# Performance work log

Measured on AMD Instinct MI355X. Metric: run time of the kernel, lower is better.

## Reference

```python
import jax, jax.numpy as jnp
from jax import lax
import numpy as np

B, A, N_CLS = 2, 3, 3          # batch, anchors per voxel, classes
D, H, W = 64, 128, 128         # 3D feature-map volume
M = 128                        # padded max GT boxes per sample
ALPHA = 2.0                    # focal exponent (module's self.alpha)
EPS = 1e-4                     # probability clamp (module's self.eps)
NMS = True                     # max-pool NMS filtering on neg mask


def setup_inputs() -> dict:
    key = jax.random.key(0)
    logits = jax.random.normal(key, (B, N_CLS * A, D, H, W), dtype=jnp.float32)
    rng = np.random.default_rng(0)
    # prob_gt: -1 = hard negative to mine, 0 = ignore, c in [1..N_CLS] = positive of class c
    prob = np.zeros((B, A, D, H, W), np.float32)
    prob[rng.random((B, A, D, H, W)) < 0.3] = -1.0
    coord = -np.ones((B, M, 4), np.int64)  # rows (a,d,h,w), -1 padded
    k = 96  # valid GT boxes per sample
    for b in range(B):
        a = rng.integers(0, A, k)
        d = rng.integers(0, D, k)
        h = rng.integers(0, H, k)
        w = rng.integers(0, W, k)
        c = rng.integers(1, N_CLS + 1, k)
        prob[b, a, d, h, w] = c
        coord[b, :k] = np.stack([a, d, h, w], 1)
    return {
        "logits": logits,
        "prob_gt": jnp.asarray(prob),
        "coord_gt": jnp.asarray(coord),
        "weight_cls": jnp.ones((N_CLS,), jnp.float32),
    }


def _per_sample(pp, cg, pg, weight_cls):
    # pp: [N_CLS, A, D, H, W] probs; cg: [M,4] int coords (-1 padded); pg: [A,D,H,W]
    valid = cg[:, 0] > -1                              # [M]
    a = jnp.where(valid, cg[:, 0], 0)
    d = jnp.where(valid, cg[:, 1], 0)
    h = jnp.where(valid, cg[:, 2], 0)
    w = jnp.where(valid, cg[:, 3], 0)
    cls = jnp.where(valid, pg[a, d, h, w].astype(jnp.int32) - 1, 0)  # [M]
    vf = valid.astype(pp.dtype)
    # positive term
    pt = pp[cls, a, d, h, w]                           # [M]
    w_pos = lax.stop_gradient(1.0 - pt) ** ALPHA * weight_cls[cls] * vf
    l_pos = -jnp.sum(jnp.log(pt) * w_pos)
    c_pos = jnp.sum(w_pos)
    # "other classes at positive locations" term
    po = pp[:, a, d, h, w]                             # [N_CLS, M]
    w_oth = lax.stop_gradient(
        jnp.maximum(po - (pt - 0.1)[None, :], 0.0)
        * (po > 0.5) * (pt > 0.5)[None, :]
    )
    # torch `weight[cls_gt] = 0` zeroes whole rows for every gt class present
    zero_rows = jnp.any((jnp.arange(N_CLS)[:, None] == cls[None, :]) & valid[None, :], axis=1)
    w_oth = jnp.where(zero_rows[:, None], 0.0, w_oth) * vf[None, :]
    l_oth = jnp.sum(-jnp.log(1.0 - po) * w_oth)
    c_oth = jnp.sum(w_oth)
    return l_pos, c_pos, l_oth, c_oth


def _focal(logits, prob_gt, coord_gt, weight_cls):
    p = jnp.clip(jax.nn.sigmoid(logits), EPS, 1.0 - EPS)  # [B, N_CLS*A, D, H, W]
    bsz, C, dd, hh, ww = logits.shape
    negmask = (prob_gt == -1).astype(p.dtype)             # [B, A, D, H, W]
    negmask = jnp.repeat(negmask[:, None], N_CLS, axis=1).reshape(p.shape)
    if NMS:
        pooled = lax.reduce_window(logits, -jnp.inf, lax.max,
                                   (1, 1, 3, 3, 3), (1, 1, 1, 1, 1), 'SAME')
        max_filter = lax.stop_gradient((pooled == logits).astype(p.dtype))
        thresh_filter = (p > EPS).astype(p.dtype)
        negmask = negmask * max_filter * thresh_filter
    w_neg = lax.stop_gradient(p) ** ALPHA * negmask
    loss_neg = -jnp.sum(jnp.log(1.0 - p) * w_neg)
    count_neg = jnp.sum(w_neg)
    p6 = p.reshape(bsz, N_CLS, C // N_CLS, dd, hh, ww)
    l_pos, c_pos, l_oth, c_oth = jax.vmap(_per_sample, in_axes=(0, 0, 0, None))(
        p6, coord_gt, prob_gt, weight_cls)
    return jnp.stack([jnp.sum(l_pos), loss_neg, jnp.sum(l_oth),
                      jnp.sum(c_pos), count_neg, jnp.sum(c_oth)])


def reference(logits, prob_gt, coord_gt, weight_cls):
    # returns [cls_loss_pos, cls_loss_neg, cls_loss_other, count_pos, count_neg, count_other]
    return _focal(logits, prob_gt, coord_gt, weight_cls)
```

## Files before the change

kernel.cpp:

```cpp
#include <hip/hip_runtime.h>
#include <cstdint>
#include <cstddef>

#define B_    2
#define A_    3
#define NCLS_ 3
#define CH_   9
#define D_    64
#define H_    128
#define W_    128
#define M_    128
#define TH    16
#define EPS_      1e-4f
#define ONE_M_EPS 0.9999f
#define NLOG2E    -1.4426950408889634f
#define LN2_      0.6931471805599453f

__device__ __forceinline__ float4 fmax4(float4 a, float4 b) {
    return make_float4(fmaxf(a.x, b.x), fmaxf(a.y, b.y),
                       fmaxf(a.z, b.z), fmaxf(a.w, b.w));
}

__device__ __forceinline__ float exp2_fast(float x) { return __builtin_amdgcn_exp2f(x); }
__device__ __forceinline__ float log2_fast(float x) { return __builtin_amdgcn_logf(x); }

__global__ __launch_bounds__(256) void neg_kernel(
    const float* __restrict__ logits, const float* __restrict__ prob,
    float* __restrict__ partials)
{
    const int gh   = blockIdx.x * 8 + (threadIdx.x >> 5);
    const int lw   = threadIdx.x & 31;
    const int lane = threadIdx.x & 63;
    const float NEG = -INFINITY;

    const int d  = gh & (D_ - 1);
    const int ht = (gh >> 6) & (H_ / TH - 1);
    const int bc = gh >> 9;
    const int b  = bc / CH_;
    const int a  = (bc - b * CH_) % A_;

    const size_t HW = (size_t)H_ * W_;
    const float* Ld = logits + ((size_t)bc * D_ + d) * HW + 4 * lw;
    const float* Pb = prob   + (((size_t)b * A_ + a) * D_ + d) * HW + 4 * lw;
    const float* Lm = (d > 0)      ? Ld - HW : Ld;
    const float* Lp = (d + 1 < D_) ? Ld + HW : Ld;
    const int h0 = ht * TH;

    struct Raw { float4 c, m, p; };
    auto issue = [&](int hh) -> Raw {
        const int hc = min(max(hh, 0), H_ - 1);
        const size_t o = (size_t)hc * W_;
        Raw r;
        r.c = *(const float4*)(Ld + o);
        r.m = *(const float4*)(Lm + o);
        r.p = *(const float4*)(Lp + o);
        return r;
    };
    auto ldpg = [&](int hh) -> float4 {
        const int hc = min(hh, H_ - 1);
        return *(const float4*)(Pb + (size_t)hc * W_);
    };

    float lacc2 = 0.0f, cacc = 0.0f;

    Raw rawP = issue(h0 - 1);
    Raw raw0 = issue(h0);
    Raw raw1 = issue(h0 + 1);
    Raw rawD = issue(h0 + 2);
    Raw rawE = issue(h0 + 3);
    float4 pgB = ldpg(h0), pgC = ldpg(h0 + 1);
    float4 pgD = ldpg(h0 + 2), pgE = ldpg(h0 + 3);

    float4 vmA = fmax4(rawP.c, fmax4(rawP.m, rawP.p));
    float4 vmB = fmax4(raw0.c, fmax4(raw0.m, raw0.p));
    float4 xB  = raw0.c;
    float4 vmC = fmax4(raw1.c, fmax4(raw1.m, raw1.p));
    float4 xC  = raw1.c;

    #pragma unroll
    for (int i = 0; i < TH; ++i) {
        const int r = h0 + i;

        Raw rawN; float4 pgN;
        if (i < TH - 4) { rawN = issue(r + 4); pgN = ldpg(r + 4); }

        const float4 vmD = fmax4(rawD.c, fmax4(rawD.m, rawD.p));
        const float4 xD  = rawD.c;

        float4 cm = fmax4(vmA, fmax4(vmB, vmC));
        const float lftv = __shfl(cm.w, (lane + 63) & 63, 64);
        const float rgtv = __shfl(cm.x, (lane + 1) & 63, 64);
        const float left  = (lw == 0)  ? NEG : lftv;
        const float right = (lw == 31) ? NEG : rgtv;
        float4 m;
        m.x = fmaxf(left, fmaxf(cm.x, cm.y));
        m.y = fmaxf(cm.x, fmaxf(cm.y, cm.z));
        m.z = fmaxf(cm.y, fmaxf(cm.z, cm.w));
        m.w = fmaxf(cm.z, fmaxf(cm.w, right));

        {
            const float x = xB.x;
            const bool pre = (pgB.x == -1.0f) & (m.x == x);
            if (__any(pre)) {
                const float u = exp2_fast(x * NLOG2E);
                const float p = __builtin_amdgcn_fmed3f(
                                    __builtin_amdgcn_rcpf(1.0f + u), EPS_, ONE_M_EPS);
                const float wn = (pre & (p > EPS_)) ? p * p : 0.0f;
                cacc += wn;
                lacc2 = fmaf(log2_fast(1.0f - p), wn, lacc2);
            }
        }
        {
            const float x = xB.y;
            const bool pre = (pgB.y == -1.0f) & (m.y == x);
            if (__any(pre)) {
                const float u = exp2_fast(x * NLOG2E);
                const float p = __builtin_amdgcn_fmed3f(
                                    __builtin_amdgcn_rcpf(1.0f + u), EPS_, ONE_M_EPS);
                const float wn = (pre & (p > EPS_)) ? p * p : 0.0f;
                cacc += wn;
                lacc2 = fmaf(log2_fast(1.0f - p), wn, lacc2);
            }
        }
        {
            const float x = xB.z;
            const bool pre = (pgB.z == -1.0f) & (m.z == x);
            if (__any(pre)) {
                const float u = exp2_fast(x * NLOG2E);
                const float p = __builtin_amdgcn_fmed3f(
                                    __builtin_amdgcn_rcpf(1.0f + u), EPS_, ONE_M_EPS);
                const float wn = (pre & (p > EPS_)) ? p * p : 0.0f;
                cacc += wn;
                lacc2 = fmaf(log2_fast(1.0f - p), wn, lacc2);
            }
        }
        {
            const float x = xB.w;
            const bool pre = (pgB.w == -1.0f) & (m.w == x);
            if (__any(pre)) {
                const float u = exp2_fast(x * NLOG2E);
                const float p = __builtin_amdgcn_fmed3f(
                                    __builtin_amdgcn_rcpf(1.0f + u), EPS_, ONE_M_EPS);
                const float wn = (pre & (p > EPS_)) ? p * p : 0.0f;
                cacc += wn;
                lacc2 = fmaf(log2_fast(1.0f - p), wn, lacc2);
            }
        }

        vmA = vmB; vmB = vmC; vmC = vmD;
        xB = xC;  xC = xD;
        pgB = pgC; pgC = pgD; pgD = pgE; pgE = pgN;
        rawD = rawE; rawE = rawN;
    }

    float lacc = lacc2 * (-LN2_);

    #pragma unroll
    for (int off = 32; off > 0; off >>= 1) {
        lacc += __shfl_down(lacc, off);
        cacc += __shfl_down(cacc, off);
    }
    __shared__ float rl[4], rc[4];
    const int wv = threadIdx.x >> 6;
    if (lane == 0) { rl[wv] = lacc; rc[wv] = cacc; }
    __syncthreads();
    if (threadIdx.x == 0) {
        partials[2 * (size_t)blockIdx.x]     = rl[0] + rl[1] + rl[2] + rl[3];
        partials[2 * (size_t)blockIdx.x + 1] = rc[0] + rc[1] + rc[2] + rc[3];
    }
}

__global__ __launch_bounds__(256) void pos_reduce_kernel(
    const float* __restrict__ logits, const float* __restrict__ prob,
    const int* __restrict__ coord, const float* __restrict__ wcls,
    const float* __restrict__ partials, int nb, float* __restrict__ out)
{
    const int tid = threadIdx.x;
    const int b = tid >> 7;
    const int m = tid & (M_ - 1);
    __shared__ int zr[B_][NCLS_];
    if (tid < B_ * NCLS_) zr[tid / NCLS_][tid % NCLS_] = 0;
    __syncthreads();

    const int* cg = coord + ((size_t)b * M_ + m) * 4;
    const int c0 = cg[0];
    const bool valid = c0 > -1;
    const int a = valid ? c0    : 0;
    const int d = valid ? cg[1] : 0;
    const int h = valid ? cg[2] : 0;
    const int w = valid ? cg[3] : 0;

    const size_t HW = (size_t)H_ * W_;
    const size_t sp = (size_t)d * HW + (size_t)h * W_ + w;

    const float pv = prob[((size_t)b * A_ + a) * D_ * HW + sp];
    const int cls = valid ? ((int)pv - 1) : 0;
    if (valid) zr[b][cls] = 1;
    __syncthreads();

    auto sigclip = [](float x) {
        float p = 1.0f / (1.0f + __expf(-x));
        return fminf(fmaxf(p, EPS_), ONE_M_EPS);
    };

    const float vf = valid ? 1.0f : 0.0f;
    const float pt = sigclip(logits[((size_t)(b * CH_ + cls * A_ + a)) * D_ * HW + sp]);
    const float wp = (1.0f - pt) * (1.0f - pt) * wcls[cls] * vf;
    float lpos = -__logf(pt) * wp;
    float cpos = wp;

    float loth = 0.0f, coth = 0.0f;
    const bool ptg = pt > 0.5f;
    #pragma unroll
    for (int cc = 0; cc < NCLS_; ++cc) {
        const float po = sigclip(logits[((size_t)(b * CH_ + cc * A_ + a)) * D_ * HW + sp]);
        float wo = fmaxf(po - (pt - 0.1f), 0.0f);
        wo = (po > 0.5f && ptg) ? wo : 0.0f;
        wo = zr[b][cc] ? 0.0f : wo;
        wo *= vf;
        loth -= __logf(1.0f - po) * wo;
        coth += wo;
    }

    float l = 0.0f, c = 0.0f;
    for (int i = tid; i < nb; i += 256) {
        l += partials[2 * (size_t)i];
        c += partials[2 * (size_t)i + 1];
    }

    #pragma unroll
    for (int off = 32; off > 0; off >>= 1) {
        lpos += __shfl_down(lpos, off);
        cpos += __shfl_down(cpos, off);
        loth += __shfl_down(loth, off);
        coth += __shfl_down(coth, off);
        l    += __shfl_down(l, off);
        c    += __shfl_down(c, off);
    }
    __shared__ float r6[4][6];
    const int lane = tid & 63, wv = tid >> 6;
    if (lane == 0) {
        r6[wv][0] = lpos; r6[wv][1] = cpos; r6[wv][2] = loth;
        r6[wv][3] = coth; r6[wv][4] = l;    r6[wv][5] = c;
    }
    __syncthreads();
    if (tid == 0) {
        out[0] = r6[0][0] + r6[1][0] + r6[2][0] + r6[3][0];
        out[3] = r6[0][1] + r6[1][1] + r6[2][1] + r6[3][1];
        out[2] = r6[0][2] + r6[1][2] + r6[2][2] + r6[3][2];
        out[5] = r6[0][3] + r6[1][3] + r6[2][3] + r6[3][3];
        out[1] = r6[0][4] + r6[1][4] + r6[2][4] + r6[3][4];
        out[4] = r6[0][5] + r6[1][5] + r6[2][5] + r6[3][5];
    }
}

extern "C" void kernel_launch(void* const* d_in, const int* in_sizes, int n_in,
                              void* d_out, int out_size, void* d_ws, size_t ws_size,
                              hipStream_t stream)
{
    const float* logits = (const float*)d_in[0];
    const float* prob   = (const float*)d_in[1];
    const int*   coord  = (const int*)d_in[2];
    const float* wcls   = (const float*)d_in[3];
    float* out = (float*)d_out;

    const int num_tiles = B_ * CH_ * D_ * (H_ / TH);
    const int nb = num_tiles / 8;

    float* partials = (float*)d_ws;

    neg_kernel<<<dim3(nb), dim3(256), 0, stream>>>(logits, prob, partials);
    pos_reduce_kernel<<<dim3(1), dim3(256), 0, stream>>>(logits, prob, coord, wcls,
                                                         partials, nb, out);
}
```

Before: 135.9 us.

## Share depth-neighbor rows via LDS across 8 consecutive depth slices per block

Each block now handles 8 consecutive depth slices of the same (b,channel,h-tile), with each half-wave loading only its own slice row and staging it in a 3-row ring buffer in shared memory. The depth-direction max is taken from neighbors in LDS instead of reloading the d-1 and d+1 rows from global memory, so global logits traffic drops from about 3x to about 1.25x. Block indices are also swizzled to change the scheduling order. The cost is two __syncthreads per row and added LDS traffic, which could stall the pipelined loads.

```diff
diff --git a/kernel.cpp b/kernel.cpp
--- a/kernel.cpp
+++ b/kernel.cpp
@@ -28,64 +28,98 @@
     const float* __restrict__ logits, const float* __restrict__ prob,
     float* __restrict__ partials)
 {
-    const int gh   = blockIdx.x * 8 + (threadIdx.x >> 5);
+    const int orig = blockIdx.x;
+    const int swz  = (orig & 7) * 144 + (orig >> 3);
+    const int hw   = threadIdx.x >> 5;
     const int lw   = threadIdx.x & 31;
     const int lane = threadIdx.x & 63;
     const float NEG = -INFINITY;
 
-    const int d  = gh & (D_ - 1);
-    const int ht = (gh >> 6) & (H_ / TH - 1);
-    const int bc = gh >> 9;
-    const int b  = bc / CH_;
-    const int a  = (bc - b * CH_) % A_;
+    const int dchunk = swz & 7;
+    int t = swz >> 3;
+    const int cls = t % 3; t /= 3;
+    const int ht  = t & 7;
+    const int ba  = t >> 3;
+    const int b = ba / 3, a = ba % 3;
+    const int bc = b * CH_ + cls * A_ + a;
+    const int d  = dchunk * 8 + hw;
+    const int h0 = ht * TH;
 
     const size_t HW = (size_t)H_ * W_;
     const float* Ld = logits + ((size_t)bc * D_ + d) * HW + 4 * lw;
     const float* Pb = prob   + (((size_t)b * A_ + a) * D_ + d) * HW + 4 * lw;
-    const float* Lm = (d > 0)      ? Ld - HW : Ld;
-    const float* Lp = (d + 1 < D_) ? Ld + HW : Ld;
-    const int h0 = ht * TH;
-
-    struct Raw { float4 c, m, p; };
-    auto issue = [&](int hh) -> Raw {
+    const bool hasE = (hw == 0) | (hw == 7);
+    const float* Le = (hw == 0) ? ((d > 0) ? Ld - HW : Ld)
+                                : ((d + 1 < D_) ? Ld + HW : Ld);
+    const int pe = (hw == 0) ? 0 : 9;
+
+    __shared__ float lds[3][10][128];
+
+    auto ldc = [&](int hh) -> float4 {
         const int hc = min(max(hh, 0), H_ - 1);
-        const size_t o = (size_t)hc * W_;
-        Raw r;
-        r.c = *(const float4*)(Ld + o);
-        r.m = *(const float4*)(Lm + o);
-        r.p = *(const float4*)(Lp + o);
-        return r;
+        return *(const float4*)(Ld + (size_t)hc * W_);
+    };
+    auto lde = [&](int hh) -> float4 {
+        const int hc = min(max(hh, 0), H_ - 1);
+        return *(const float4*)(Le + (size_t)hc * W_);
     };
     auto ldpg = [&](int hh) -> float4 {
         const int hc = min(hh, H_ - 1);
         return *(const float4*)(Pb + (size_t)hc * W_);
     };
-
-    float lacc2 = 0.0f, cacc = 0.0f;
-
-    Raw rawP = issue(h0 - 1);
-    Raw raw0 = issue(h0);
-    Raw raw1 = issue(h0 + 1);
-    Raw rawD = issue(h0 + 2);
-    Raw rawE = issue(h0 + 3);
+    auto ST = [&](int s, float4 c, float4 e) {
+        *(float4*)&lds[s][hw + 1][4 * lw] = c;
+        if (hasE) *(float4*)&lds[s][pe][4 * lw] = e;
+    };
+    auto VM = [&](int s, float4 own) -> float4 {
+        const float4 x = *(const float4*)&lds[s][hw][4 * lw];
+        const float4 y = *(const float4*)&lds[s][hw + 2][4 * lw];
+        return fmax4(own, fmax4(x, y));
+    };
+
+    const int base = h0 % 3;
+    const int s_0  = base;
+    const int s_p1 = (base + 1 == 3) ? 0 : base + 1;
+    const int s_m1 = (base == 0) ? 2 : base - 1;
+
+    float4 cA = ldc(h0 - 1);
+    float4 cB = ldc(h0), cC = ldc(h0 + 1), cD = ldc(h0 + 2), cE = ldc(h0 + 3);
+    float4 eA, eB, eC, eD, eE;
+    if (hasE) {
+        eA = lde(h0 - 1); eB = lde(h0); eC = lde(h0 + 1);
+        eD = lde(h0 + 2); eE = lde(h0 + 3);
+    }
     float4 pgB = ldpg(h0), pgC = ldpg(h0 + 1);
     float4 pgD = ldpg(h0 + 2), pgE = ldpg(h0 + 3);
 
-    float4 vmA = fmax4(rawP.c, fmax4(rawP.m, rawP.p));
-    float4 vmB = fmax4(raw0.c, fmax4(raw0.m, raw0.p));
-    float4 xB  = raw0.c;
-    float4 vmC = fmax4(raw1.c, fmax4(raw1.m, raw1.p));
-    float4 xC  = raw1.c;
+    ST(s_m1, cA, eA);
+    ST(s_0,  cB, eB);
+    ST(s_p1, cC, eC);
+    __syncthreads();
+    float4 vmA = VM(s_m1, cA);
+    float4 vmB = VM(s_0,  cB);
+    float4 vmC = VM(s_p1, cC);
+    __syncthreads();
+
+    float lacc2 = 0.0f, cacc = 0.0f;
+    int sW = s_m1;
 
     #pragma unroll
     for (int i = 0; i < TH; ++i) {
         const int r = h0 + i;
 
-        Raw rawN; float4 pgN;
-        if (i < TH - 4) { rawN = issue(r + 4); pgN = ldpg(r + 4); }
-
-        const float4 vmD = fmax4(rawD.c, fmax4(rawD.m, rawD.p));
-        const float4 xD  = rawD.c;
+        if (i != TH - 1) ST(sW, cD, eD);
+        __syncthreads();
+
+        float4 cN, eN, pgN;
+        if (i <= TH - 4) {
+            cN = ldc(r + 4);
+            if (hasE) eN = lde(r + 4);
+            pgN = ldpg(r + 4);
+        }
+
+        float4 vmN;
+        if (i != TH - 1) vmN = VM(sW, cD);
 
         float4 cm = fmax4(vmA, fmax4(vmB, vmC));
         const float lftv = __shfl(cm.w, (lane + 63) & 63, 64);
@@ -99,7 +133,7 @@
         m.w = fmaxf(cm.z, fmaxf(cm.w, right));
 
         {
-            const float x = xB.x;
+            const float x = cB.x;
             const bool pre = (pgB.x == -1.0f) & (m.x == x);
             if (__any(pre)) {
                 const float u = exp2_fast(x * NLOG2E);
@@ -111,7 +145,7 @@
             }
         }
         {
-            const float x = xB.y;
+            const float x = cB.y;
             const bool pre = (pgB.y == -1.0f) & (m.y == x);
             if (__any(pre)) {
                 const float u = exp2_fast(x * NLOG2E);
@@ -123,7 +157,7 @@
             }
         }
         {
-            const float x = xB.z;
+            const float x = cB.z;
             const bool pre = (pgB.z == -1.0f) & (m.z == x);
             if (__any(pre)) {
                 const float u = exp2_fast(x * NLOG2E);
@@ -135,7 +169,7 @@
             }
         }
         {
-            const float x = xB.w;
+            const float x = cB.w;
             const bool pre = (pgB.w == -1.0f) & (m.w == x);
             if (__any(pre)) {
                 const float u = exp2_fast(x * NLOG2E);
@@ -147,10 +181,11 @@
             }
         }
 
-        vmA = vmB; vmB = vmC; vmC = vmD;
-        xB = xC;  xC = xD;
+        vmA = vmB; vmB = vmC; vmC = vmN;
+        cB = cC; cC = cD; cD = cE; cE = cN;
+        if (hasE) { eB = eC; eC = eD; eD = eE; eE = eN; }
         pgB = pgC; pgC = pgD; pgD = pgE; pgE = pgN;
-        rawD = rawE; rawE = rawN;
+        sW = (sW + 1 == 3) ? 0 : sW + 1;
     }
 
     float lacc = lacc2 * (-LN2_);
@@ -264,8 +299,7 @@
     const float* wcls   = (const float*)d_in[3];
     float* out = (float*)d_out;
 
-    const int num_tiles = B_ * CH_ * D_ * (H_ / TH);
-    const int nb = num_tiles / 8;
+    const int nb = B_ * CH_ * (D_ / 8) * (H_ / TH);
 
     float* partials = (float*)d_ws;
 
```

After: 146.5 us. 7.8% more time.

## Stream NMS window along depth with cross-wave row sharing and block swizzle

Applied to the files above, without the earlier changes.

Reorganizes the 3x3x3 max-pool kernel so each wavefront covers two adjacent H rows and marches along D instead of along H. The H-neighbor max comes from a cross-half lane shuffle plus one extra edge-row load, replacing the three depth-plane loads per row. A block-index swizzle is added to spread neighboring tiles across the grid. The aim is less redundant global traffic per output, at the cost of extra shuffles and a changed access order.

```diff
diff --git a/kernel.cpp b/kernel.cpp
--- a/kernel.cpp
+++ b/kernel.cpp
@@ -10,7 +10,7 @@
 #define H_    128
 #define W_    128
 #define M_    128
-#define TH    16
+#define TD    16
 #define EPS_      1e-4f
 #define ONE_M_EPS 0.9999f
 #define NLOG2E    -1.4426950408889634f
@@ -24,70 +24,81 @@
 __device__ __forceinline__ float exp2_fast(float x) { return __builtin_amdgcn_exp2f(x); }
 __device__ __forceinline__ float log2_fast(float x) { return __builtin_amdgcn_logf(x); }
 
+struct Raw { float4 c, e, pg; };
+
 __global__ __launch_bounds__(256) void neg_kernel(
     const float* __restrict__ logits, const float* __restrict__ prob,
     float* __restrict__ partials)
 {
-    const int gh   = blockIdx.x * 8 + (threadIdx.x >> 5);
-    const int lw   = threadIdx.x & 31;
-    const int lane = threadIdx.x & 63;
+    const int orig = blockIdx.x;
+    const int swz  = (orig & 7) * 144 + (orig >> 3);
+    const int tid  = threadIdx.x;
+    const int lw   = tid & 31;
+    const int lane = tid & 63;
+    const int hwi  = tid >> 5;
+    const int half = hwi & 1;
     const float NEG = -INFINITY;
 
-    const int d  = gh & (D_ - 1);
-    const int ht = (gh >> 6) & (H_ / TH - 1);
-    const int bc = gh >> 9;
-    const int b  = bc / CH_;
-    const int a  = (bc - b * CH_) % A_;
+    const int htile  = swz & 15;
+    const int dchunk = (swz >> 4) & 3;
+    const int bc     = swz >> 6;
+    const int b = bc / CH_;
+    const int a = (bc - b * CH_) % A_;
+    const int d0 = dchunk * TD;
+    const int r  = htile * 8 + hwi;
+    const int er = half ? min(r + 1, H_ - 1) : max(r - 1, 0);
 
     const size_t HW = (size_t)H_ * W_;
-    const float* Ld = logits + ((size_t)bc * D_ + d) * HW + 4 * lw;
-    const float* Pb = prob   + (((size_t)b * A_ + a) * D_ + d) * HW + 4 * lw;
-    const float* Lm = (d > 0)      ? Ld - HW : Ld;
-    const float* Lp = (d + 1 < D_) ? Ld + HW : Ld;
-    const int h0 = ht * TH;
-
-    struct Raw { float4 c, m, p; };
-    auto issue = [&](int hh) -> Raw {
-        const int hc = min(max(hh, 0), H_ - 1);
-        const size_t o = (size_t)hc * W_;
-        Raw r;
-        r.c = *(const float4*)(Ld + o);
-        r.m = *(const float4*)(Lm + o);
-        r.p = *(const float4*)(Lp + o);
-        return r;
-    };
-    auto ldpg = [&](int hh) -> float4 {
-        const int hc = min(hh, H_ - 1);
-        return *(const float4*)(Pb + (size_t)hc * W_);
-    };
+    const float* Cb = logits + (size_t)bc * D_ * HW + (size_t)r  * W_ + 4 * lw;
+    const float* Eb = logits + (size_t)bc * D_ * HW + (size_t)er * W_ + 4 * lw;
+    const float* Pb = prob + (size_t)(b * A_ + a) * D_ * HW + (size_t)r * W_ + 4 * lw;
+
+    auto ldc = [&](int dq) -> float4 {
+        const int dc = min(max(dq, 0), D_ - 1);
+        return *(const float4*)(Cb + (size_t)dc * HW);
+    };
+    auto lde = [&](int dq) -> float4 {
+        const int dc = min(max(dq, 0), D_ - 1);
+        return *(const float4*)(Eb + (size_t)dc * HW);
+    };
+    auto ldpg = [&](int dq) -> float4 {
+        const int dc = min(max(dq, 0), D_ - 1);
+        return *(const float4*)(Pb + (size_t)dc * HW);
+    };
+    auto shfl4 = [&](float4 v) -> float4 {
+        const int p = lane ^ 32;
+        return make_float4(__shfl(v.x, p, 64), __shfl(v.y, p, 64),
+                           __shfl(v.z, p, 64), __shfl(v.w, p, 64));
+    };
+    auto hv = [&](const Raw& rw) -> float4 {
+        return fmax4(rw.c, fmax4(rw.e, shfl4(rw.c)));
+    };
+
+    Raw rm1; rm1.c = ldc(d0 - 1); rm1.e = lde(d0 - 1);
+    Raw r0;  r0.c  = ldc(d0);     r0.e  = lde(d0);     r0.pg  = ldpg(d0);
+    Raw rawD; rawD.c = ldc(d0+1); rawD.e = lde(d0+1);  rawD.pg = ldpg(d0+1);
+    Raw rawE; rawE.c = ldc(d0+2); rawE.e = lde(d0+2);  rawE.pg = ldpg(d0+2);
+
+    float4 hwmA = hv(rm1);
+    float4 hwmB = hv(r0);
+    float4 xc   = r0.c;
+    float4 pgc  = r0.pg;
 
     float lacc2 = 0.0f, cacc = 0.0f;
 
-    Raw rawP = issue(h0 - 1);
-    Raw raw0 = issue(h0);
-    Raw raw1 = issue(h0 + 1);
-    Raw rawD = issue(h0 + 2);
-    Raw rawE = issue(h0 + 3);
-    float4 pgB = ldpg(h0), pgC = ldpg(h0 + 1);
-    float4 pgD = ldpg(h0 + 2), pgE = ldpg(h0 + 3);
-
-    float4 vmA = fmax4(rawP.c, fmax4(rawP.m, rawP.p));
-    float4 vmB = fmax4(raw0.c, fmax4(raw0.m, raw0.p));
-    float4 xB  = raw0.c;
-    float4 vmC = fmax4(raw1.c, fmax4(raw1.m, raw1.p));
-    float4 xC  = raw1.c;
-
-    #pragma unroll
-    for (int i = 0; i < TH; ++i) {
-        const int r = h0 + i;
-
-        Raw rawN; float4 pgN;
-        if (i < TH - 4) { rawN = issue(r + 4); pgN = ldpg(r + 4); }
-
-        const float4 vmD = fmax4(rawD.c, fmax4(rawD.m, rawD.p));
-        const float4 xD  = rawD.c;
-
-        float4 cm = fmax4(vmA, fmax4(vmB, vmC));
+    #pragma unroll
+    for (int j = 0; j < TD; ++j) {
+        Raw rawN = rawE;
+        if (j <= TD - 3) {
+            rawN.c = ldc(d0 + j + 3); rawN.e = lde(d0 + j + 3);
+            rawN.pg = ldpg(d0 + j + 3);
+        }
+
+        const float4 hwmC = hv(rawD);
+        const float4 xN   = rawD.c;
+        const float4 pgN  = rawD.pg;
+
+        float4 cm = fmax4(hwmA, fmax4(hwmB, hwmC));
         const float lftv = __shfl(cm.w, (lane + 63) & 63, 64);
         const float rgtv = __shfl(cm.x, (lane + 1) & 63, 64);
         const float left  = (lw == 0)  ? NEG : lftv;
@@ -99,57 +110,56 @@
         m.w = fmaxf(cm.z, fmaxf(cm.w, right));
 
         {
-            const float x = xB.x;
-            const bool pre = (pgB.x == -1.0f) & (m.x == x);
-            if (__any(pre)) {
-                const float u = exp2_fast(x * NLOG2E);
-                const float p = __builtin_amdgcn_fmed3f(
-                                    __builtin_amdgcn_rcpf(1.0f + u), EPS_, ONE_M_EPS);
-                const float wn = (pre & (p > EPS_)) ? p * p : 0.0f;
-                cacc += wn;
-                lacc2 = fmaf(log2_fast(1.0f - p), wn, lacc2);
-            }
-        }
-        {
-            const float x = xB.y;
-            const bool pre = (pgB.y == -1.0f) & (m.y == x);
-            if (__any(pre)) {
-                const float u = exp2_fast(x * NLOG2E);
-                const float p = __builtin_amdgcn_fmed3f(
-                                    __builtin_amdgcn_rcpf(1.0f + u), EPS_, ONE_M_EPS);
-                const float wn = (pre & (p > EPS_)) ? p * p : 0.0f;
-                cacc += wn;
-                lacc2 = fmaf(log2_fast(1.0f - p), wn, lacc2);
-            }
-        }
-        {
-            const float x = xB.z;
-            const bool pre = (pgB.z == -1.0f) & (m.z == x);
-            if (__any(pre)) {
-                const float u = exp2_fast(x * NLOG2E);
-                const float p = __builtin_amdgcn_fmed3f(
-                                    __builtin_amdgcn_rcpf(1.0f + u), EPS_, ONE_M_EPS);
-                const float wn = (pre & (p > EPS_)) ? p * p : 0.0f;
-                cacc += wn;
-                lacc2 = fmaf(log2_fast(1.0f - p), wn, lacc2);
-            }
-        }
-        {
-            const float x = xB.w;
-            const bool pre = (pgB.w == -1.0f) & (m.w == x);
-            if (__any(pre)) {
-                const float u = exp2_fast(x * NLOG2E);
-                const float p = __builtin_amdgcn_fmed3f(
-                                    __builtin_amdgcn_rcpf(1.0f + u), EPS_, ONE_M_EPS);
-                const float wn = (pre & (p > EPS_)) ? p * p : 0.0f;
-                cacc += wn;
-                lacc2 = fmaf(log2_fast(1.0f - p), wn, lacc2);
-            }
-        }
-
-        vmA = vmB; vmB = vmC; vmC = vmD;
-        xB = xC;  xC = xD;
-        pgB = pgC; pgC = pgD; pgD = pgE; pgE = pgN;
+            const float x = xc.x;
+            const bool pre = (pgc.x == -1.0f) & (m.x == x);
+            if (__any(pre)) {
+                const float u = exp2_fast(x * NLOG2E);
+                const float p = __builtin_amdgcn_fmed3f(
+                                    __builtin_amdgcn_rcpf(1.0f + u), EPS_, ONE_M_EPS);
+                const float wn = (pre & (p > EPS_)) ? p * p : 0.0f;
+                cacc += wn;
+                lacc2 = fmaf(log2_fast(1.0f - p), wn, lacc2);
+            }
+        }
+        {
+            const float x = xc.y;
+            const bool pre = (pgc.y == -1.0f) & (m.y == x);
+            if (__any(pre)) {
+                const float u = exp2_fast(x * NLOG2E);
+                const float p = __builtin_amdgcn_fmed3f(
+                                    __builtin_amdgcn_rcpf(1.0f + u), EPS_, ONE_M_EPS);
+                const float wn = (pre & (p > EPS_)) ? p * p : 0.0f;
+                cacc += wn;
+                lacc2 = fmaf(log2_fast(1.0f - p), wn, lacc2);
+            }
+        }
+        {
+            const float x = xc.z;
+            const bool pre = (pgc.z == -1.0f) & (m.z == x);
+            if (__any(pre)) {
+                const float u = exp2_fast(x * NLOG2E);
+                const float p = __builtin_amdgcn_fmed3f(
+                                    __builtin_amdgcn_rcpf(1.0f + u), EPS_, ONE_M_EPS);
+                const float wn = (pre & (p > EPS_)) ? p * p : 0.0f;
+                cacc += wn;
+                lacc2 = fmaf(log2_fast(1.0f - p), wn, lacc2);
+            }
+        }
+        {
+            const float x = xc.w;
+            const bool pre = (pgc.w == -1.0f) & (m.w == x);
+            if (__any(pre)) {
+                const float u = exp2_fast(x * NLOG2E);
+                const float p = __builtin_amdgcn_fmed3f(
+                                    __builtin_amdgcn_rcpf(1.0f + u), EPS_, ONE_M_EPS);
+                const float wn = (pre & (p > EPS_)) ? p * p : 0.0f;
+                cacc += wn;
+                lacc2 = fmaf(log2_fast(1.0f - p), wn, lacc2);
+            }
+        }
+
+        hwmA = hwmB; hwmB = hwmC;
+        xc = xN; pgc = pgN;
         rawD = rawE; rawE = rawN;
     }
 
@@ -264,8 +274,7 @@
     const float* wcls   = (const float*)d_in[3];
     float* out = (float*)d_out;
 
-    const int num_tiles = B_ * CH_ * D_ * (H_ / TH);
-    const int nb = num_tiles / 8;
+    const int nb = B_ * CH_ * (H_ / 8) * (D_ / TD);
 
     float* partials = (float*)d_ws;
 
```

Result: slower. 138.6 us (+2.0%).
